# Kernel optimization log

Measured on AMD Instinct MI355X. Metric: run time of the kernel, lower is better.

The kernel has to match this reference:

```python
import jax, jax.numpy as jnp
import numpy as np

B, S, E, H = 2, 2048, 1024, 16
D = E // H  # head_dim = 64


def setup_inputs() -> dict:
    key = jax.random.key(0)
    ks = jax.random.split(key, 12)
    s = 1.0 / np.sqrt(E)
    return {
        "queries": jax.random.normal(ks[0], (B, S, E), jnp.float32),
        "keys": jax.random.normal(ks[1], (B, S, E), jnp.float32),
        "values": jax.random.normal(ks[2], (B, S, E), jnp.float32),
        "mask": jnp.zeros((B, 1, S, S), jnp.float32),
        "Wq": jax.random.normal(ks[3], (E, E), jnp.float32) * s,
        "bq": jnp.zeros((E,), jnp.float32),
        "Wk": jax.random.normal(ks[4], (E, E), jnp.float32) * s,
        "bk": jnp.zeros((E,), jnp.float32),
        "Wv": jax.random.normal(ks[5], (E, E), jnp.float32) * s,
        "bv": jnp.zeros((E,), jnp.float32),
        "Wo": jax.random.normal(ks[6], (E, E), jnp.float32) * s,
        "bo": jnp.zeros((E,), jnp.float32),
    }


def reference(queries, keys, values, mask, Wq, bq, Wk, bk, Wv, bv, Wo, bo):
    # QKV projections, then split heads: [B,S,E] -> [B,H,S,D]
    def split_heads(x):
        return x.reshape(B, S, H, D).transpose(0, 2, 1, 3)

    Q = split_heads(queries @ Wq + bq)
    K = split_heads(keys @ Wk + bk)
    V = split_heads(values @ Wv + bv)
    scale = jnp.sqrt(jnp.asarray(D, jnp.float32))
    # [B,H,S,S] attention scores
    scores = jnp.einsum("bhqd,bhkd->bhqk", Q, K) / scale
    scores = scores + mask * -10000.0
    weights = jax.nn.softmax(scores, axis=-1)
    # [B,H,S,D] -> [B,S,E]
    out = jnp.einsum("bhqk,bhkd->bhqd", weights, V)
    out = out.transpose(0, 2, 1, 3).reshape(B, S, E)
    return out @ Wo + bo
```

## Files before the change

kernel.cpp:

```cpp
#include <hip/hip_runtime.h>
#include <hip/hip_bf16.h>
#include <stdint.h>

#define B_ 2
#define S_ 2048
#define E_ 1024
#define H_ 16
#define D_ 64
#define LOG2E 1.4426950408889634f

typedef unsigned short ubf;
typedef __attribute__((ext_vector_type(8))) short bh8;
typedef __attribute__((ext_vector_type(4))) float fx4;
typedef __attribute__((ext_vector_type(16))) float fx16;

__device__ __forceinline__ ubf f2bf(float f) {
  unsigned u = __float_as_uint(f);
  unsigned r = (u + 0x7fffu + ((u >> 16) & 1u)) >> 16;
  return (ubf)r;
}

__device__ __forceinline__ unsigned cvtpk(float lo, float hi2) {
  unsigned r;
  asm("v_cvt_pk_bf16_f32 %0, %1, %2" : "=v"(r) : "v"(lo), "v"(hi2));
  return r;
}

__device__ __forceinline__ void pl32swap(unsigned& a, unsigned& b) {
  asm("v_permlane32_swap_b32 %0, %1" : "+v"(a), "+v"(b));
}

__device__ __forceinline__ void gl_lds16(const void* g, void* l) {
  __builtin_amdgcn_global_load_lds(
      (const __attribute__((address_space(1))) void*)g,
      (__attribute__((address_space(3))) void*)l, 16, 0, 0);
}

__global__ void cvt3(const float* __restrict__ q, const float* __restrict__ k,
                     const float* __restrict__ v, ubf* __restrict__ dst0,
                     int* __restrict__ flag) {
  if (blockIdx.x == 0 && blockIdx.z == 0 && threadIdx.x == 0) *flag = 0;
  const float* src = (blockIdx.z == 0) ? q : (blockIdx.z == 1) ? k : v;
  ubf* dst = dst0 + (size_t)blockIdx.z * (B_ * S_ * E_);
  int n4 = (B_ * S_ * E_) / 4;
  int stride = gridDim.x * blockDim.x;
  for (int j = blockIdx.x * blockDim.x + threadIdx.x; j < n4; j += stride) {
    float4 x = ((const float4*)src)[j];
    ushort4 o;
    o.x = f2bf(x.x); o.y = f2bf(x.y); o.z = f2bf(x.z); o.w = f2bf(x.w);
    ((ushort4*)dst)[j] = o;
  }
}

__global__ void wtrans4(const float* __restrict__ Wq, const float* __restrict__ Wk,
                        const float* __restrict__ Wv, const float* __restrict__ Wo,
                        ubf* __restrict__ Wt0) {
  __shared__ float t[32][33];
  int z = blockIdx.z;
  const float* W = (z == 0) ? Wq : (z == 1) ? Wk : (z == 2) ? Wv : Wo;
  ubf* Wt = Wt0 + (size_t)z * (E_ * E_);
  int kb = blockIdx.x, nb = blockIdx.y;
  int c = threadIdx.x & 31, r0 = threadIdx.x >> 5;
#pragma unroll
  for (int rr = 0; rr < 32; rr += 8)
    t[r0 + rr][c] = W[(size_t)(kb * 32 + r0 + rr) * E_ + nb * 32 + c];
  __syncthreads();
#pragma unroll
  for (int rr = 0; rr < 32; rr += 8)
    Wt[(size_t)(nb * 32 + r0 + rr) * E_ + kb * 32 + c] = f2bf(t[c][r0 + rr]);
}

__global__ void maskscan(const float* __restrict__ m, int n4, int* __restrict__ flag) {
  int stride = gridDim.x * blockDim.x;
  int any = 0;
  for (int j = blockIdx.x * blockDim.x + threadIdx.x; j < n4; j += stride) {
    float4 x = ((const float4*)m)[j];
    any |= (x.x != 0.f) | (x.y != 0.f) | (x.z != 0.f) | (x.w != 0.f);
  }
  if (any) atomicOr(flag, 1);
}

__global__ void __launch_bounds__(256)
gemm_qkv(const ubf* __restrict__ X, const ubf* __restrict__ Wt,
         const float* __restrict__ bq, const float* __restrict__ bk,
         const float* __restrict__ bv, ubf* __restrict__ Out) {
  constexpr int K = 1024;
  __shared__ ubf Asm[2][128 * 32];
  __shared__ ubf Bsm[2][128 * 32];
  const int z = blockIdx.z;
  const ubf* A  = (z == 2) ? (Wt + 2u * 1048576u) : (X + (size_t)z * 4194304u);
  const ubf* Bt = (z == 2) ? (X + 2u * 4194304u) : (Wt + (size_t)z * 1048576u);
  const float* bias = (z == 0) ? bq : (z == 1) ? bk : bv;
  ubf* Cout = Out + (size_t)z * 4194304u;
  const int bm = (z == 2) ? blockIdx.y : blockIdx.x;
  const int bn = (z == 2) ? blockIdx.x : blockIdx.y;

  const int tid = threadIdx.x;
  const int lane = tid & 63, w = tid >> 6;
  const int wm = w >> 1, wn = w & 1;
  const int g = lane >> 4, c15 = lane & 15;

  const fx4 FZ = {0.f, 0.f, 0.f, 0.f};
  fx4 acc[4][4];
#pragma unroll
  for (int m = 0; m < 4; m++)
#pragma unroll
    for (int n = 0; n < 4; n++) acc[m][n] = FZ;

  auto stage = [&](int buf, int k0) {
#pragma unroll
    for (int i = 0; i < 2; i++) {
      int s = i * 256 + tid;
      int row = s >> 2, cc = s & 3;
      int sc = cc ^ (row & 3);
      gl_lds16(A + (size_t)(bm * 128 + row) * K + k0 + sc * 8,
               (char*)&Asm[buf][0] + (i * 256 + (tid & 192)) * 16);
      gl_lds16(Bt + (size_t)(bn * 128 + row) * K + k0 + sc * 8,
               (char*)&Bsm[buf][0] + (i * 256 + (tid & 192)) * 16);
    }
  };

  stage(0, 0);
  __syncthreads();
  for (int t = 0; t < K / 32; t++) {
    int cur = t & 1;
    if (t + 1 < K / 32) stage(cur ^ 1, (t + 1) * 32);
    bh8 a[4], b[4];
#pragma unroll
    for (int m = 0; m < 4; m++) {
      int row = wm * 64 + m * 16 + c15;
      int ch = g ^ (row & 3);
      a[m] = *(const bh8*)((const char*)&Asm[cur][0] + row * 64 + ch * 16);
    }
#pragma unroll
    for (int n = 0; n < 4; n++) {
      int row = wn * 64 + n * 16 + c15;
      int ch = g ^ (row & 3);
      b[n] = *(const bh8*)((const char*)&Bsm[cur][0] + row * 64 + ch * 16);
    }
#pragma unroll
    for (int m = 0; m < 4; m++)
#pragma unroll
      for (int n = 0; n < 4; n++)
        acc[m][n] = __builtin_amdgcn_mfma_f32_16x16x32_bf16(a[m], b[n], acc[m][n], 0, 0, 0);
    __syncthreads();
  }

#pragma unroll
  for (int m = 0; m < 4; m++) {
    int rbase = bm * 128 + wm * 64 + m * 16 + g * 4;
#pragma unroll
    for (int n = 0; n < 4; n++) {
      int col = bn * 128 + wn * 64 + n * 16 + c15;
#pragma unroll
      for (int r = 0; r < 4; r++) {
        int mrow = rbase + r;
        float val = acc[m][n][r];
        if (z <= 1) {
          val = val + bias[col];
          if (z == 0) val *= 0.125f * LOG2E;
          int bb = mrow >> 11, ss = mrow & 2047, hh = col >> 6, dd = col & 63;
          Cout[((size_t)(bb * H_ + hh) * S_ + ss) * D_ + dd] = f2bf(val);
        } else {
          val = val + bias[mrow];
          int bb = col >> 11, ss = col & 2047, hh = mrow >> 6, dd = mrow & 63;
          Cout[((size_t)(bb * H_ + hh) * D_ + dd) * S_ + ss] = f2bf(val);
        }
      }
    }
  }
}

__global__ void __launch_bounds__(256)
gemm_out(const ubf* __restrict__ A, const ubf* __restrict__ Bt,
         const float* __restrict__ bias, float* __restrict__ Cout, int N) {
  constexpr int K = 1024;
  __shared__ ubf Asm[2][128 * 32];
  __shared__ ubf Bsm[2][128 * 32];
  const int tid = threadIdx.x;
  const int lane = tid & 63, w = tid >> 6;
  const int wm = w >> 1, wn = w & 1;
  const int bm = blockIdx.y, bn = blockIdx.x;
  const int g = lane >> 4, c15 = lane & 15;

  const fx4 FZ = {0.f, 0.f, 0.f, 0.f};
  fx4 acc[4][4];
#pragma unroll
  for (int m = 0; m < 4; m++)
#pragma unroll
    for (int n = 0; n < 4; n++) acc[m][n] = FZ;

  auto stage = [&](int buf, int k0) {
#pragma unroll
    for (int i = 0; i < 2; i++) {
      int s = i * 256 + tid;
      int row = s >> 2, cc = s & 3;
      int sc = cc ^ (row & 3);
      gl_lds16(A + (size_t)(bm * 128 + row) * K + k0 + sc * 8,
               (char*)&Asm[buf][0] + (i * 256 + (tid & 192)) * 16);
      gl_lds16(Bt + (size_t)(bn * 128 + row) * K + k0 + sc * 8,
               (char*)&Bsm[buf][0] + (i * 256 + (tid & 192)) * 16);
    }
  };

  stage(0, 0);
  __syncthreads();
  for (int t = 0; t < K / 32; t++) {
    int cur = t & 1;
    if (t + 1 < K / 32) stage(cur ^ 1, (t + 1) * 32);
    bh8 a[4], b[4];
#pragma unroll
    for (int m = 0; m < 4; m++) {
      int row = wm * 64 + m * 16 + c15;
      int ch = g ^ (row & 3);
      a[m] = *(const bh8*)((const char*)&Asm[cur][0] + row * 64 + ch * 16);
    }
#pragma unroll
    for (int n = 0; n < 4; n++) {
      int row = wn * 64 + n * 16 + c15;
      int ch = g ^ (row & 3);
      b[n] = *(const bh8*)((const char*)&Bsm[cur][0] + row * 64 + ch * 16);
    }
#pragma unroll
    for (int m = 0; m < 4; m++)
#pragma unroll
      for (int n = 0; n < 4; n++)
        acc[m][n] = __builtin_amdgcn_mfma_f32_16x16x32_bf16(a[m], b[n], acc[m][n], 0, 0, 0);
    __syncthreads();
  }

#pragma unroll
  for (int m = 0; m < 4; m++) {
    int rbase = bm * 128 + wm * 64 + m * 16 + g * 4;
#pragma unroll
    for (int n = 0; n < 4; n++) {
      int col = bn * 128 + wn * 64 + n * 16 + c15;
#pragma unroll
      for (int r = 0; r < 4; r++)
        Cout[(size_t)(rbase + r) * N + col] = acc[m][n][r] + bias[col];
    }
  }
}

#define ROWQ(r) (((r) & 3) + 8 * ((r) >> 2) + 4 * hi)

#define PV_STEP(KF, W0, W1, W2, W3)                                             \
    {                                                                           \
      unsigned wa[4] = {W0, W1, W2, W3};                                        \
      bh8 pa = *(bh8*)wa;                                                       \
      int ch = (2 * (KF) + hi) ^ (l31 & 7);                                     \
      bh8 bv0 = *(const bh8*)(Vc + l31 * 128 + ch * 16);                        \
      acc0 = __builtin_amdgcn_mfma_f32_32x32x16_bf16(pa, bv0, acc0, 0, 0, 0);   \
      bh8 bv1 = *(const bh8*)(Vc + (32 + l31) * 128 + ch * 16);                 \
      acc1 = __builtin_amdgcn_mfma_f32_32x32x16_bf16(pa, bv1, acc1, 0, 0, 0);   \
    }

__global__ void __launch_bounds__(256, 4)
flash_fast(const ubf* __restrict__ Q, const ubf* __restrict__ Kh,
           const ubf* __restrict__ Vt, float* __restrict__ O0,
           float* __restrict__ O1, float2* __restrict__ ml) {
  __shared__ ubf Ksm[2][64 * 64];
  __shared__ ubf Vsm[2][64 * 64];
  const int tid = threadIdx.x, lane = tid & 63, w = tid >> 6;
  const int l31 = lane & 31, hi = lane >> 5;
  const int bh = blockIdx.x;
  const int qb = blockIdx.y;
  const int half = blockIdx.z;
  const int qg = qb * 128 + w * 32 + l31;
  const int k00 = half * (S_ / 2);
  constexpr int NT = (S_ / 2) / 64;

  const ubf* Qrow = Q + ((size_t)bh * S_ + qg) * D_;
  bh8 q4[4];
#pragma unroll
  for (int kf = 0; kf < 4; kf++) q4[kf] = *(const bh8*)(Qrow + kf * 16 + hi * 8);

  fx16 acc0, acc1;
#pragma unroll
  for (int i = 0; i < 16; i++) { acc0[i] = 0.f; acc1[i] = 0.f; }
  float lrun = 0.f;

  const ubf* Kg = Kh + (size_t)bh * S_ * D_;
  const ubf* Vg = Vt + (size_t)bh * D_ * S_;

  auto stage = [&](int buf, int k0) {
#pragma unroll
    for (int i = 0; i < 2; i++) {
      int s = i * 256 + tid;
      int row = s >> 3, cc = s & 7;
      int sw = cc ^ (row & 7);
      gl_lds16(Kg + (size_t)(k0 + row) * D_ + sw * 8,
               (char*)&Ksm[buf][0] + (i * 256 + (tid & 192)) * 16);
      gl_lds16(Vg + (size_t)row * S_ + k0 + sw * 8,
               (char*)&Vsm[buf][0] + (i * 256 + (tid & 192)) * 16);
    }
  };

  stage(0, k00);
  __syncthreads();

  for (int t = 0; t < NT; t++) {
    int cur = t & 1;
    if (t + 1 < NT) stage(cur ^ 1, k00 + (t + 1) * 64);
    const char* Kc = (const char*)&Ksm[cur][0];
    const char* Vc = (const char*)&Vsm[cur][0];

#pragma unroll
    for (int h2 = 0; h2 < 2; h2++) {
      fx16 sc;
#pragma unroll
      for (int i = 0; i < 16; i++) sc[i] = 0.f;
      __builtin_amdgcn_s_setprio(1);
#pragma unroll
      for (int kf = 0; kf < 4; kf++) {
        int ch = (2 * kf + hi) ^ (l31 & 7);
        bh8 ak = *(const bh8*)(Kc + (h2 * 32 + l31) * 128 + ch * 16);
        sc = __builtin_amdgcn_mfma_f32_32x32x16_bf16(ak, q4[kf], sc, 0, 0, 0);
      }
      __builtin_amdgcn_s_setprio(0);

      float rsv[4] = {0.f, 0.f, 0.f, 0.f};
#pragma unroll
      for (int i = 0; i < 16; i++) {
        float p = exp2f(sc[i]);
        sc[i] = p;
        rsv[i & 3] += p;
      }
      lrun += (rsv[0] + rsv[1]) + (rsv[2] + rsv[3]);

      unsigned pk[8];
#pragma unroll
      for (int i = 0; i < 8; i++) pk[i] = cvtpk(sc[2 * i], sc[2 * i + 1]);
      pl32swap(pk[0], pk[2]); pl32swap(pk[1], pk[3]);
      pl32swap(pk[4], pk[6]); pl32swap(pk[5], pk[7]);

      __builtin_amdgcn_s_setprio(1);
      PV_STEP(2 * h2,     pk[0], pk[1], pk[2], pk[3])
      PV_STEP(2 * h2 + 1, pk[4], pk[5], pk[6], pk[7])
      __builtin_amdgcn_s_setprio(0);
    }
    __syncthreads();
  }

  float lsum = lrun + __shfl_xor(lrun, 32);
  float* Obase = half ? O1 : O0;
#pragma unroll
  for (int r = 0; r < 16; r++) {
    int q2 = ROWQ(r);
    size_t rowbase = ((size_t)bh * S_ + qb * 128 + w * 32 + q2) * D_;
    Obase[rowbase + l31] = acc0[r];
    Obase[rowbase + 32 + l31] = acc1[r];
  }
  if (hi == 0) {
    int sq = qb * 128 + w * 32 + l31;
    ml[(size_t)half * (32 * S_) + bh * S_ + sq] = make_float2(0.0f, lsum);
  }
}

__global__ void __launch_bounds__(256)
combine(const float* __restrict__ O0, const float* __restrict__ O1,
        const float2* __restrict__ ml, ubf* __restrict__ AO) {
  int tid = blockIdx.x * 256 + threadIdx.x;
  int row = tid >> 4, dq = tid & 15;
  int bh = row >> 11, s = row & 2047;
  float2 m0 = ml[row];
  float2 m1 = ml[32 * S_ + row];
  float m = fmaxf(m0.x, m1.x);
  float w0 = exp2f(m0.x - m), w1 = exp2f(m1.x - m);
  float inv = 1.0f / (m0.y * w0 + m1.y * w1);
  float4 a = *(const float4*)(O0 + (size_t)row * D_ + dq * 4);
  float4 c = *(const float4*)(O1 + (size_t)row * D_ + dq * 4);
  ushort4 o;
  o.x = f2bf((a.x * w0 + c.x * w1) * inv);
  o.y = f2bf((a.y * w0 + c.y * w1) * inv);
  o.z = f2bf((a.z * w0 + c.z * w1) * inv);
  o.w = f2bf((a.w * w0 + c.w * w1) * inv);
  int b_ = bh >> 4, h = bh & 15;
  *(ushort4*)(AO + ((size_t)(b_ * S_ + s)) * E_ + h * 64 + dq * 4) = o;
}

__global__ void __launch_bounds__(256, 4)
flash_masked(const ubf* __restrict__ Q, const ubf* __restrict__ Kh,
             const ubf* __restrict__ Vt, const float* __restrict__ mask,
             const int* __restrict__ flag, ubf* __restrict__ AO) {
  if (*flag == 0) return;
  __shared__ ubf Ksm[2][64 * 64];
  __shared__ ubf Vsm[2][64 * 64];
  const int tid = threadIdx.x, lane = tid & 63, w = tid >> 6;
  const int l31 = lane & 31, hi = lane >> 5;
  const int bh = blockIdx.x;
  const int qb = blockIdx.y;
  const int b = bh >> 4, h = bh & 15;
  const int qg = qb * 128 + w * 32 + l31;
  constexpr int NT = S_ / 64;

  const ubf* Qrow = Q + ((size_t)bh * S_ + qg) * D_;
  bh8 q4[4];
#pragma unroll
  for (int kf = 0; kf < 4; kf++) q4[kf] = *(const bh8*)(Qrow + kf * 16 + hi * 8);

  fx16 acc0, acc1;
#pragma unroll
  for (int i = 0; i < 16; i++) { acc0[i] = 0.f; acc1[i] = 0.f; }
  float mrun = -3.0e38f, lrun = 0.f;

  const ubf* Kg = Kh + (size_t)bh * S_ * D_;
  const ubf* Vg = Vt + (size_t)bh * D_ * S_;

  auto stage = [&](int buf, int k0) {
#pragma unroll
    for (int i = 0; i < 2; i++) {
      int s = i * 256 + tid;
      int row = s >> 3, cc = s & 7;
      int sw = cc ^ (row & 7);
      gl_lds16(Kg + (size_t)(k0 + row) * D_ + sw * 8,
               (char*)&Ksm[buf][0] + (i * 256 + (tid & 192)) * 16);
      gl_lds16(Vg + (size_t)row * S_ + k0 + sw * 8,
               (char*)&Vsm[buf][0] + (i * 256 + (tid & 192)) * 16);
    }
  };

  stage(0, 0);
  __syncthreads();

  for (int t = 0; t < NT; t++) {
    int cur = t & 1;
    if (t + 1 < NT) stage(cur ^ 1, (t + 1) * 64);
    const char* Kc = (const char*)&Ksm[cur][0];
    const char* Vc = (const char*)&Vsm[cur][0];

#pragma unroll
    for (int h2 = 0; h2 < 2; h2++) {
      fx16 sc;
#pragma unroll
      for (int i = 0; i < 16; i++) sc[i] = 0.f;
#pragma unroll
      for (int kf = 0; kf < 4; kf++) {
        int ch = (2 * kf + hi) ^ (l31 & 7);
        bh8 ak = *(const bh8*)(Kc + (h2 * 32 + l31) * 128 + ch * 16);
        sc = __builtin_amdgcn_mfma_f32_32x32x16_bf16(ak, q4[kf], sc, 0, 0, 0);
      }
      const float* mq = mask + ((size_t)(b * S_ + qg)) * S_ + t * 64 + h2 * 32;
#pragma unroll
      for (int r = 0; r < 16; r++)
        sc[r] += mq[ROWQ(r)] * (-14426.950408889634f);

      float pm = sc[0];
#pragma unroll
      for (int r = 1; r < 16; r++) pm = fmaxf(pm, sc[r]);
      pm = fmaxf(pm, __shfl_xor(pm, 32));
      if (__any(pm - mrun > 11.5415603f)) {
        float mnew = fmaxf(mrun, pm);
        float al = exp2f(mrun - mnew);
        lrun *= al;
#pragma unroll
        for (int r = 0; r < 16; r++) {
          float alr = __shfl(al, ROWQ(r));
          acc0[r] *= alr;
          acc1[r] *= alr;
        }
        mrun = mnew;
      }
      float rsv[4] = {0.f, 0.f, 0.f, 0.f};
#pragma unroll
      for (int i = 0; i < 16; i++) {
        float p = exp2f(sc[i] - mrun);
        sc[i] = p;
        rsv[i & 3] += p;
      }
      lrun += (rsv[0] + rsv[1]) + (rsv[2] + rsv[3]);

      unsigned pk[8];
#pragma unroll
      for (int i = 0; i < 8; i++) pk[i] = cvtpk(sc[2 * i], sc[2 * i + 1]);
      pl32swap(pk[0], pk[2]); pl32swap(pk[1], pk[3]);
      pl32swap(pk[4], pk[6]); pl32swap(pk[5], pk[7]);

      PV_STEP(2 * h2,     pk[0], pk[1], pk[2], pk[3])
      PV_STEP(2 * h2 + 1, pk[4], pk[5], pk[6], pk[7])
    }
    __syncthreads();
  }

  float ltot = lrun + __shfl_xor(lrun, 32);
#pragma unroll
  for (int r = 0; r < 16; r++) {
    int q2 = ROWQ(r);
    float linv = 1.0f / __shfl(ltot, q2);
    size_t base = ((size_t)(b * S_ + qb * 128 + w * 32 + q2)) * E_ + h * 64;
    AO[base + l31] = f2bf(acc0[r] * linv);
    AO[base + 32 + l31] = f2bf(acc1[r] * linv);
  }
}

extern "C" void kernel_launch(void* const* d_in, const int* in_sizes, int n_in,
                              void* d_out, int out_size, void* d_ws, size_t ws_size,
                              hipStream_t stream) {
  (void)in_sizes; (void)n_in; (void)out_size; (void)ws_size;
  const float* q  = (const float*)d_in[0];
  const float* k  = (const float*)d_in[1];
  const float* v  = (const float*)d_in[2];
  const float* mask = (const float*)d_in[3];
  const float* Wq = (const float*)d_in[4];
  const float* bq = (const float*)d_in[5];
  const float* Wk = (const float*)d_in[6];
  const float* bk = (const float*)d_in[7];
  const float* Wv = (const float*)d_in[8];
  const float* bv = (const float*)d_in[9];
  const float* Wo = (const float*)d_in[10];
  const float* bo = (const float*)d_in[11];

  char* ws = (char*)d_ws;
  ubf* X    = (ubf*)(ws);
  ubf* Wt0  = (ubf*)(ws + 25165824);
  ubf* Qh   = (ubf*)(ws + 33554432);
  ubf* Kh   = (ubf*)(ws + 41943040);
  ubf* Vt   = (ubf*)(ws + 50331648);
  ubf* AO   = (ubf*)(ws + 58720256);
  int* flag = (int*)(ws + 67108864);
  float*  O0p = (float*)(ws);
  float2* mlp = (float2*)(ws + 16777216);
  float*  O1p = (float*)d_out;

  ubf* Wot = Wt0 + 3145728;

  cvt3<<<dim3(512, 1, 3), 256, 0, stream>>>(q, k, v, X, flag);
  wtrans4<<<dim3(32, 32, 4), 256, 0, stream>>>(Wq, Wk, Wv, Wo, Wt0);
  maskscan<<<1024, 256, 0, stream>>>(mask, (B_ * S_ * S_) / 4, flag);

  gemm_qkv<<<dim3(32, 8, 3), 256, 0, stream>>>(X, Wt0, bq, bk, bv, Qh);

  flash_fast<<<dim3(32, 16, 2), 256, 0, stream>>>(Qh, Kh, Vt, O0p, O1p, mlp);
  combine<<<4096, 256, 0, stream>>>(O0p, O1p, mlp, AO);
  flash_masked<<<dim3(32, 16), 256, 0, stream>>>(Qh, Kh, Vt, mask, flag, AO);

  gemm_out<<<dim3(8, 32), 256, 0, stream>>>(AO, Wot, bo, (float*)d_out, 1024);
}
```

Before: 165.4 us.

## Fuse mask scan into prep kernel and loosen flash_fast tile synchronization

The mask scan now runs as a fourth z-slice of the bf16 conversion kernel. It writes per-wave flags instead of an atomic, and flash_masked reduces those flags itself, which removes one launch and the flag reset. In flash_fast, the double-buffered K/V staging replaces __syncthreads with explicit vmcnt waits plus a raw s_barrier, so the next tile's loads stay in flight while the current tile computes. It also seeds the first MFMA with a zero register and splits the row-sum accumulator into two chains. The hand-written waitcnt counts must exactly match the number of outstanding global-to-LDS loads, or a wave may read stale LDS.

Result: no change. 164.6 us (-0.5%).

```diff
diff --git a/kernel.cpp b/kernel.cpp
--- a/kernel.cpp
+++ b/kernel.cpp
@@ -36,15 +36,27 @@
       (__attribute__((address_space(3))) void*)l, 16, 0, 0);
 }
 
-__global__ void cvt3(const float* __restrict__ q, const float* __restrict__ k,
-                     const float* __restrict__ v, ubf* __restrict__ dst0,
-                     int* __restrict__ flag) {
-  if (blockIdx.x == 0 && blockIdx.z == 0 && threadIdx.x == 0) *flag = 0;
-  const float* src = (blockIdx.z == 0) ? q : (blockIdx.z == 1) ? k : v;
-  ubf* dst = dst0 + (size_t)blockIdx.z * (B_ * S_ * E_);
-  int n4 = (B_ * S_ * E_) / 4;
-  int stride = gridDim.x * blockDim.x;
-  for (int j = blockIdx.x * blockDim.x + threadIdx.x; j < n4; j += stride) {
+__global__ void prep(const float* __restrict__ q, const float* __restrict__ k,
+                     const float* __restrict__ v, const float* __restrict__ mask,
+                     ubf* __restrict__ dst0, int* __restrict__ flagarr) {
+  const int z = blockIdx.z;
+  const int tid = threadIdx.x;
+  const int stride = gridDim.x * blockDim.x;
+  if (z == 3) {
+    int any = 0;
+    const int n4m = (B_ * S_ * S_) / 4;
+    for (int j = blockIdx.x * blockDim.x + tid; j < n4m; j += stride) {
+      float4 x = ((const float4*)mask)[j];
+      any |= (x.x != 0.f) | (x.y != 0.f) | (x.z != 0.f) | (x.w != 0.f);
+    }
+    int wany = __any(any != 0) ? 1 : 0;
+    if ((tid & 63) == 0) flagarr[blockIdx.x * 4 + (tid >> 6)] = wany;
+    return;
+  }
+  const float* src = (z == 0) ? q : (z == 1) ? k : v;
+  ubf* dst = dst0 + (size_t)z * (B_ * S_ * E_);
+  const int n4 = (B_ * S_ * E_) / 4;
+  for (int j = blockIdx.x * blockDim.x + tid; j < n4; j += stride) {
     float4 x = ((const float4*)src)[j];
     ushort4 o;
     o.x = f2bf(x.x); o.y = f2bf(x.y); o.z = f2bf(x.z); o.w = f2bf(x.w);
@@ -68,16 +80,6 @@
 #pragma unroll
   for (int rr = 0; rr < 32; rr += 8)
     Wt[(size_t)(nb * 32 + r0 + rr) * E_ + kb * 32 + c] = f2bf(t[c][r0 + rr]);
-}
-
-__global__ void maskscan(const float* __restrict__ m, int n4, int* __restrict__ flag) {
-  int stride = gridDim.x * blockDim.x;
-  int any = 0;
-  for (int j = blockIdx.x * blockDim.x + threadIdx.x; j < n4; j += stride) {
-    float4 x = ((const float4*)m)[j];
-    any |= (x.x != 0.f) | (x.y != 0.f) | (x.z != 0.f) | (x.w != 0.f);
-  }
-  if (any) atomicOr(flag, 1);
 }
 
 __global__ void __launch_bounds__(256)
@@ -275,10 +277,10 @@
 #pragma unroll
   for (int kf = 0; kf < 4; kf++) q4[kf] = *(const bh8*)(Qrow + kf * 16 + hi * 8);
 
-  fx16 acc0, acc1;
-#pragma unroll
-  for (int i = 0; i < 16; i++) { acc0[i] = 0.f; acc1[i] = 0.f; }
-  float lrun = 0.f;
+  fx16 acc0, acc1, ZF;
+#pragma unroll
+  for (int i = 0; i < 16; i++) { acc0[i] = 0.f; acc1[i] = 0.f; ZF[i] = 0.f; }
+  float2 lr2 = make_float2(0.f, 0.f);
 
   const ubf* Kg = Kh + (size_t)bh * S_ * D_;
   const ubf* Vg = Vt + (size_t)bh * D_ * S_;
@@ -297,36 +299,43 @@
   };
 
   stage(0, k00);
-  __syncthreads();
 
   for (int t = 0; t < NT; t++) {
     int cur = t & 1;
-    if (t + 1 < NT) stage(cur ^ 1, k00 + (t + 1) * 64);
+    if (t + 1 < NT) {
+      stage(cur ^ 1, k00 + (t + 1) * 64);
+      asm volatile("s_waitcnt vmcnt(4)" ::: "memory");
+    } else {
+      asm volatile("s_waitcnt vmcnt(0)" ::: "memory");
+    }
+    __builtin_amdgcn_s_barrier();
     const char* Kc = (const char*)&Ksm[cur][0];
     const char* Vc = (const char*)&Vsm[cur][0];
 
 #pragma unroll
     for (int h2 = 0; h2 < 2; h2++) {
       fx16 sc;
-#pragma unroll
-      for (int i = 0; i < 16; i++) sc[i] = 0.f;
       __builtin_amdgcn_s_setprio(1);
-#pragma unroll
-      for (int kf = 0; kf < 4; kf++) {
+      {
+        int ch = hi ^ (l31 & 7);
+        bh8 ak = *(const bh8*)(Kc + (h2 * 32 + l31) * 128 + ch * 16);
+        sc = __builtin_amdgcn_mfma_f32_32x32x16_bf16(ak, q4[0], ZF, 0, 0, 0);
+      }
+#pragma unroll
+      for (int kf = 1; kf < 4; kf++) {
         int ch = (2 * kf + hi) ^ (l31 & 7);
         bh8 ak = *(const bh8*)(Kc + (h2 * 32 + l31) * 128 + ch * 16);
         sc = __builtin_amdgcn_mfma_f32_32x32x16_bf16(ak, q4[kf], sc, 0, 0, 0);
       }
       __builtin_amdgcn_s_setprio(0);
 
-      float rsv[4] = {0.f, 0.f, 0.f, 0.f};
-#pragma unroll
-      for (int i = 0; i < 16; i++) {
-        float p = exp2f(sc[i]);
-        sc[i] = p;
-        rsv[i & 3] += p;
-      }
-      lrun += (rsv[0] + rsv[1]) + (rsv[2] + rsv[3]);
+#pragma unroll
+      for (int i = 0; i < 8; i++) {
+        float p0 = exp2f(sc[2 * i]);
+        float p1 = exp2f(sc[2 * i + 1]);
+        sc[2 * i] = p0; sc[2 * i + 1] = p1;
+        lr2.x += p0; lr2.y += p1;
+      }
 
       unsigned pk[8];
 #pragma unroll
@@ -339,9 +348,10 @@
       PV_STEP(2 * h2 + 1, pk[4], pk[5], pk[6], pk[7])
       __builtin_amdgcn_s_setprio(0);
     }
-    __syncthreads();
-  }
-
+    __builtin_amdgcn_s_barrier();
+  }
+
+  float lrun = lr2.x + lr2.y;
   float lsum = lrun + __shfl_xor(lrun, 32);
   float* Obase = half ? O1 : O0;
 #pragma unroll
@@ -382,8 +392,19 @@
 __global__ void __launch_bounds__(256, 4)
 flash_masked(const ubf* __restrict__ Q, const ubf* __restrict__ Kh,
              const ubf* __restrict__ Vt, const float* __restrict__ mask,
-             const int* __restrict__ flag, ubf* __restrict__ AO) {
-  if (*flag == 0) return;
+             const int* __restrict__ flagarr, ubf* __restrict__ AO) {
+  __shared__ int anyf;
+  if (threadIdx.x == 0) anyf = 0;
+  __syncthreads();
+  {
+    int a = 0;
+#pragma unroll
+    for (int i = 0; i < 8; i++) a |= flagarr[threadIdx.x + i * 256];
+    if (a) anyf = 1;
+  }
+  __syncthreads();
+  if (anyf == 0) return;
+
   __shared__ ubf Ksm[2][64 * 64];
   __shared__ ubf Vsm[2][64 * 64];
   const int tid = threadIdx.x, lane = tid & 63, w = tid >> 6;
@@ -517,22 +538,21 @@
   ubf* Kh   = (ubf*)(ws + 41943040);
   ubf* Vt   = (ubf*)(ws + 50331648);
   ubf* AO   = (ubf*)(ws + 58720256);
-  int* flag = (int*)(ws + 67108864);
+  int* flagarr = (int*)(ws + 67108864);
   float*  O0p = (float*)(ws);
   float2* mlp = (float2*)(ws + 16777216);
   float*  O1p = (float*)d_out;
 
   ubf* Wot = Wt0 + 3145728;
 
-  cvt3<<<dim3(512, 1, 3), 256, 0, stream>>>(q, k, v, X, flag);
+  prep<<<dim3(512, 1, 4), 256, 0, stream>>>(q, k, v, mask, X, flagarr);
   wtrans4<<<dim3(32, 32, 4), 256, 0, stream>>>(Wq, Wk, Wv, Wo, Wt0);
-  maskscan<<<1024, 256, 0, stream>>>(mask, (B_ * S_ * S_) / 4, flag);
 
   gemm_qkv<<<dim3(32, 8, 3), 256, 0, stream>>>(X, Wt0, bq, bk, bv, Qh);
 
   flash_fast<<<dim3(32, 16, 2), 256, 0, stream>>>(Qh, Kh, Vt, O0p, O1p, mlp);
   combine<<<4096, 256, 0, stream>>>(O0p, O1p, mlp, AO);
-  flash_masked<<<dim3(32, 16), 256, 0, stream>>>(Qh, Kh, Vt, mask, flag, AO);
+  flash_masked<<<dim3(32, 16), 256, 0, stream>>>(Qh, Kh, Vt, mask, flagarr, AO);
 
   gemm_out<<<dim3(8, 32), 256, 0, stream>>>(AO, Wot, bo, (float*)d_out, 1024);
 }
```
